# Kernel optimization log

Measured on AMD Instinct MI355X. Metric: run time of the kernel, lower is better.

## Reference

```python
import jax, jax.numpy as jnp
import numpy as np

B, N, D_IN, D_H, D_OUT = 32768, 8, 256, 512, 256
LN_EPS = 1e-5


def setup_inputs() -> dict:
    key = jax.random.key(0)
    ks = jax.random.split(key, 9)
    s = lambda fan_in: 1.0 / np.sqrt(fan_in)
    return {
        "state": jax.random.normal(ks[0], (B, D_IN), dtype=jnp.float32),
        "neighbor_states": jax.random.normal(ks[1], (N, B, D_IN), dtype=jnp.float32),
        "ln_gamma": jnp.ones((D_IN,), jnp.float32),
        "ln_beta": jnp.zeros((D_IN,), jnp.float32),
        "W1": jax.random.uniform(ks[2], (D_IN, D_H), jnp.float32, -s(D_IN), s(D_IN)),
        "b1": jax.random.uniform(ks[3], (D_H,), jnp.float32, -s(D_IN), s(D_IN)),
        "W2": jax.random.uniform(ks[4], (D_H, D_OUT), jnp.float32, -s(D_H), s(D_H)),
        "b2": jax.random.uniform(ks[5], (D_OUT,), jnp.float32, -s(D_H), s(D_H)),
        "attn_w": jax.random.uniform(ks[6], (D_OUT,), jnp.float32, -s(D_OUT), s(D_OUT)),
        "attn_b": jax.random.uniform(ks[7], (), jnp.float32, -s(D_OUT), s(D_OUT)),
    }


def reference(state, neighbor_states, ln_gamma, ln_beta, W1, b1, W2, b2, attn_w, attn_b):
    def process(x):
        # LayerNorm over last dim (eps=1e-5, elementwise affine)
        mu = jnp.mean(x, axis=-1, keepdims=True)
        var = jnp.mean(jnp.square(x - mu), axis=-1, keepdims=True)
        xn = (x - mu) * jax.lax.rsqrt(var + LN_EPS) * ln_gamma + ln_beta
        # Linear -> (Dropout=identity in eval) -> ReLU -> Linear
        h = jax.nn.relu(xn @ W1 + b1)
        return h @ W2 + b2

    local = process(state)                      # [B, D_OUT]
    nf = process(neighbor_states)               # [N, B, D_OUT]
    # attention aggregation: scores over neighbor axis (torch stacks at dim=1)
    scores = jnp.einsum("nbo,o->nb", nf, attn_w) + attn_b   # [N, B]
    weights = jax.nn.softmax(scores, axis=0)                  # softmax over neighbors
    agg = jnp.einsum("nbo,nb->bo", nf, weights)              # [B, D_OUT]
    return local + agg
```

## Files before the change

### kernel.cpp

```cpp
#include <hip/hip_runtime.h>
#include <hip/hip_bf16.h>
#include <math.h>

#define BROWS 32768
#define NNB   8
#define DIN   256
#define DH    512
#define DOUT  256
#define MROWS 128
#define CH    32
#define NCHUNK 16
#define SA    264
#define SH    40

typedef __attribute__((ext_vector_type(8))) short bfrag;
typedef __attribute__((ext_vector_type(4))) float ffrag;
typedef __attribute__((ext_vector_type(4))) float f4v;

__device__ __forceinline__ short f2bf(float f) {
    union { float f; unsigned u; } v; v.f = f;
    unsigned r = v.u + 0x7fffu + ((v.u >> 16) & 1u);
    return (short)(r >> 16);
}

__global__ void tcast_g(const float* __restrict__ src, const float* __restrict__ g,
                        short* __restrict__ dst, int R, int C) {
    __shared__ short t[64][67];
    const int c0 = blockIdx.x * 64, r0 = blockIdx.y * 64;
    const int lr = threadIdx.x >> 6, lc = threadIdx.x & 63;
    #pragma unroll
    for (int i = 0; i < 16; ++i) {
        int row = i * 4 + lr;
        t[row][lc] = f2bf(src[(size_t)(r0 + row) * C + c0 + lc] * g[r0 + row]);
    }
    __syncthreads();
    #pragma unroll
    for (int i = 0; i < 16; ++i) {
        int row = i * 4 + lr;
        dst[(size_t)(c0 + row) * R + r0 + lc] = t[lc][row];
    }
}

__global__ void tcast(const float* __restrict__ src, short* __restrict__ dst,
                      int R, int C) {
    __shared__ short t[64][67];
    const int c0 = blockIdx.x * 64, r0 = blockIdx.y * 64;
    const int lr = threadIdx.x >> 6, lc = threadIdx.x & 63;
    #pragma unroll
    for (int i = 0; i < 16; ++i) {
        int row = i * 4 + lr;
        t[row][lc] = f2bf(src[(size_t)(r0 + row) * C + c0 + lc]);
    }
    __syncthreads();
    #pragma unroll
    for (int i = 0; i < 16; ++i) {
        int row = i * 4 + lr;
        dst[(size_t)(c0 + row) * R + r0 + lc] = t[lc][row];
    }
}

__global__ void b1prep(const float* __restrict__ W1, const float* __restrict__ b1,
                       const float* __restrict__ beta, float* __restrict__ b1p) {
    int n = blockIdx.x * 256 + threadIdx.x;
    float acc = b1[n];
    for (int k = 0; k < DIN; ++k) acc += beta[k] * W1[(size_t)k * DH + n];
    b1p[n] = acc;
}

__global__ __launch_bounds__(512, 2)
void fused_node(const float* __restrict__ state, const float* __restrict__ nbr,
                const float* __restrict__ b1p, const float* __restrict__ b2g,
                const float* __restrict__ awg, const float* __restrict__ abg,
                const short* __restrict__ w1t, const short* __restrict__ w2t,
                float* __restrict__ out) {
    __shared__ short w1_lds[2][CH * SA];
    __shared__ short w2_lds[2][DOUT * SH];
    __shared__ short h_lds[MROWS * SH];
    __shared__ float b1_lds[DH];
    __shared__ float scorep[4 * MROWS];
    __shared__ float m_lds[MROWS], l_lds[MROWS], al_lds[MROWS], pp_lds[MROWS], il_lds[MROWS];

    const int tid = threadIdx.x;
    const int wv = tid >> 6, lane = tid & 63;
    const int q = lane >> 4, l16 = lane & 15;
    const int rg = wv >> 2, cg = wv & 3;
    const int row0 = blockIdx.x * MROWS;
    const int myrow = 16 * wv + l16;

    const int f0 = tid, f1 = tid + 512;
    const int w1r0 = f0 >> 5, w1c0 = f0 & 31, w1r1 = f1 >> 5, w1c1 = f1 & 31;
    const int w2r0 = f0 >> 2, w2c0 = f0 & 3,  w2r1 = f1 >> 2, w2c1 = f1 & 3;

    bfrag L1a = *(const bfrag*)(w1t + (size_t)f0 * 8);
    bfrag L1b = *(const bfrag*)(w1t + (size_t)f1 * 8);
    bfrag L2a = *(const bfrag*)(w2t + (size_t)w2r0 * DH + w2c0 * 8);
    bfrag L2b = *(const bfrag*)(w2t + (size_t)w2r1 * DH + w2c1 * 8);
    if (tid < DH) b1_lds[tid] = b1p[tid];
    if (tid < MROWS) { m_lds[tid] = -__builtin_huge_valf(); l_lds[tid] = 0.f; }
    *(bfrag*)(&w1_lds[0][w1r0 * SA + w1c0 * 8]) = L1a;
    *(bfrag*)(&w1_lds[0][w1r1 * SA + w1c1 * 8]) = L1b;
    *(bfrag*)(&w2_lds[0][w2r0 * SH + w2c0 * 8]) = L2a;
    *(bfrag*)(&w2_lds[0][w2r1 * SH + w2c1 * 8]) = L2b;

    float b2v[4], awv[4];
    #pragma unroll
    for (int ct = 0; ct < 4; ++ct) {
        int col = 64 * cg + 16 * ct + l16;
        b2v[ct] = b2g[col];
        awv[ct] = awg[col];
    }
    const float attnb = abg[0];

    ffrag agg[4][4];
    #pragma unroll
    for (int mt = 0; mt < 4; ++mt)
        #pragma unroll
        for (int ct = 0; ct < 4; ++ct) { ffrag z = {0.f,0.f,0.f,0.f}; agg[mt][ct] = z; }

    ffrag feat[4][4];
    bfrag xnf[8];

    for (int s = 0; s < 9; ++s) {
        const bool loc = (s == 8);
        const float* xb = loc ? (state + (size_t)row0 * DIN)
                              : (nbr + ((size_t)s * BROWS + (size_t)row0) * DIN);
        {
            const float* xr = xb + (size_t)myrow * DIN + q * 8;
            f4v xa[8], xc[8];
            #pragma unroll
            for (int kb = 0; kb < 8; ++kb) {
                xa[kb] = __builtin_nontemporal_load((const f4v*)(xr + kb * 32));
                xc[kb] = __builtin_nontemporal_load((const f4v*)(xr + kb * 32 + 4));
            }
            float sum = 0.f, ssq = 0.f;
            #pragma unroll
            for (int kb = 0; kb < 8; ++kb) {
                #pragma unroll
                for (int j = 0; j < 4; ++j) {
                    sum += xa[kb][j] + xc[kb][j];
                    ssq = fmaf(xa[kb][j], xa[kb][j], fmaf(xc[kb][j], xc[kb][j], ssq));
                }
            }
            sum += __shfl_xor(sum, 16); sum += __shfl_xor(sum, 32);
            ssq += __shfl_xor(ssq, 16); ssq += __shfl_xor(ssq, 32);
            float mean = sum * (1.f / 256.f);
            float var = ssq * (1.f / 256.f) - mean * mean;
            float rstd = rsqrtf(var + 1e-5f);
            #pragma unroll
            for (int kb = 0; kb < 8; ++kb) {
                bfrag t;
                #pragma unroll
                for (int j = 0; j < 4; ++j) {
                    t[j]     = f2bf((xa[kb][j] - mean) * rstd);
                    t[j + 4] = f2bf((xc[kb][j] - mean) * rstd);
                }
                xnf[kb] = t;
            }
        }
        #pragma unroll
        for (int mt = 0; mt < 4; ++mt)
            #pragma unroll
            for (int ct = 0; ct < 4; ++ct) {
                ffrag fi = {b2v[ct], b2v[ct], b2v[ct], b2v[ct]};
                feat[mt][ct] = fi;
            }

        for (int c = 0; c < NCHUNK; ++c) {
            const int p = c & 1;
            __syncthreads();
            const bool more = (c < NCHUNK - 1) || (s < 8);
            const int nc = (c + 1) & (NCHUNK - 1);
            if (more) {
                const short* s1 = w1t + (size_t)nc * CH * DIN;
                const short* s2 = w2t + nc * CH;
                L1a = *(const bfrag*)(s1 + (size_t)f0 * 8);
                L1b = *(const bfrag*)(s1 + (size_t)f1 * 8);
                L2a = *(const bfrag*)(s2 + (size_t)w2r0 * DH + w2c0 * 8);
                L2b = *(const bfrag*)(s2 + (size_t)w2r1 * DH + w2c1 * 8);
            }
            {
                float bb0 = b1_lds[c * CH + l16], bb1 = b1_lds[c * CH + 16 + l16];
                ffrag h0 = {bb0, bb0, bb0, bb0};
                ffrag h1 = {bb1, bb1, bb1, bb1};
                const short* bp = &w1_lds[p][l16 * SA + q * 8];
                #pragma unroll
                for (int kb = 0; kb < 8; ++kb) {
                    bfrag v0 = *(const bfrag*)(bp + kb * 32);
                    bfrag v1 = *(const bfrag*)(bp + 16 * SA + kb * 32);
                    h0 = __builtin_amdgcn_mfma_f32_16x16x32_bf16(xnf[kb], v0, h0, 0, 0, 0);
                    h1 = __builtin_amdgcn_mfma_f32_16x16x32_bf16(xnf[kb], v1, h1, 0, 0, 0);
                }
                short* hb = h_lds + (16 * wv + 4 * q) * SH + l16;
                #pragma unroll
                for (int r = 0; r < 4; ++r) {
                    hb[r * SH]      = f2bf(fmaxf(h0[r], 0.f));
                    hb[r * SH + 16] = f2bf(fmaxf(h1[r], 0.f));
                }
            }
            if (more) {
                *(bfrag*)(&w1_lds[1 - p][w1r0 * SA + w1c0 * 8]) = L1a;
                *(bfrag*)(&w1_lds[1 - p][w1r1 * SA + w1c1 * 8]) = L1b;
                *(bfrag*)(&w2_lds[1 - p][w2r0 * SH + w2c0 * 8]) = L2a;
                *(bfrag*)(&w2_lds[1 - p][w2r1 * SH + w2c1 * 8]) = L2b;
            }
            __syncthreads();
            {
                bfrag af[4], bfr[4];
                #pragma unroll
                for (int mt = 0; mt < 4; ++mt)
                    af[mt] = *(const bfrag*)(h_lds + (64 * rg + 16 * mt + l16) * SH + q * 8);
                #pragma unroll
                for (int ct = 0; ct < 4; ++ct)
                    bfr[ct] = *(const bfrag*)(&w2_lds[p][(64 * cg + 16 * ct + l16) * SH + q * 8]);
                #pragma unroll
                for (int mt = 0; mt < 4; ++mt)
                    #pragma unroll
                    for (int ct = 0; ct < 4; ++ct)
                        feat[mt][ct] = __builtin_amdgcn_mfma_f32_16x16x32_bf16(af[mt], bfr[ct], feat[mt][ct], 0, 0, 0);
            }
        }

        if (!loc) {
            float sp[4][4];
            #pragma unroll
            for (int mt = 0; mt < 4; ++mt)
                #pragma unroll
                for (int r = 0; r < 4; ++r) {
                    float vv = feat[mt][0][r] * awv[0] + feat[mt][1][r] * awv[1]
                             + feat[mt][2][r] * awv[2] + feat[mt][3][r] * awv[3];
                    vv += __shfl_xor(vv, 1); vv += __shfl_xor(vv, 2);
                    vv += __shfl_xor(vv, 4); vv += __shfl_xor(vv, 8);
                    sp[mt][r] = vv;
                }
            if (l16 == 0) {
                #pragma unroll
                for (int mt = 0; mt < 4; ++mt)
                    #pragma unroll
                    for (int r = 0; r < 4; ++r)
                        scorep[cg * MROWS + 64 * rg + 16 * mt + 4 * q + r] = sp[mt][r];
            }
            __syncthreads();
            if (tid < MROWS) {
                float sc = scorep[tid] + scorep[MROWS + tid] + scorep[2 * MROWS + tid]
                         + scorep[3 * MROWS + tid] + attnb;
                float mo = m_lds[tid];
                float mn = fmaxf(mo, sc);
                float al = __expf(mo - mn);
                float pp = __expf(sc - mn);
                float ln = l_lds[tid] * al + pp;
                m_lds[tid] = mn; l_lds[tid] = ln;
                al_lds[tid] = al; pp_lds[tid] = pp;
                if (s == NNB - 1) il_lds[tid] = 1.f / ln;
            }
            __syncthreads();
            #pragma unroll
            for (int mt = 0; mt < 4; ++mt) {
                float alv[4], ppv[4];
                #pragma unroll
                for (int r = 0; r < 4; ++r) {
                    int rr = 64 * rg + 16 * mt + 4 * q + r;
                    alv[r] = al_lds[rr]; ppv[r] = pp_lds[rr];
                }
                #pragma unroll
                for (int ct = 0; ct < 4; ++ct)
                    #pragma unroll
                    for (int r = 0; r < 4; ++r)
                        agg[mt][ct][r] = agg[mt][ct][r] * alv[r] + ppv[r] * feat[mt][ct][r];
            }
        }
    }

    #pragma unroll
    for (int mt = 0; mt < 4; ++mt)
        #pragma unroll
        for (int r = 0; r < 4; ++r) {
            int rr = 64 * rg + 16 * mt + 4 * q + r;
            float il = il_lds[rr];
            size_t base = (size_t)(row0 + rr) * DOUT + 64 * cg + l16;
            #pragma unroll
            for (int ct = 0; ct < 4; ++ct)
                __builtin_nontemporal_store(feat[mt][ct][r] + agg[mt][ct][r] * il,
                                            out + base + ct * 16);
        }
}

extern "C" void kernel_launch(void* const* d_in, const int* in_sizes, int n_in,
                              void* d_out, int out_size, void* d_ws, size_t ws_size,
                              hipStream_t stream) {
    const float* state = (const float*)d_in[0];
    const float* nbr   = (const float*)d_in[1];
    const float* gamma = (const float*)d_in[2];
    const float* beta  = (const float*)d_in[3];
    const float* W1    = (const float*)d_in[4];
    const float* b1    = (const float*)d_in[5];
    const float* W2    = (const float*)d_in[6];
    const float* b2    = (const float*)d_in[7];
    const float* aw    = (const float*)d_in[8];
    const float* ab    = (const float*)d_in[9];
    float* out = (float*)d_out;

    short* w1t = (short*)d_ws;
    short* w2t = w1t + (size_t)DH * DIN;
    float* b1p = (float*)(w2t + (size_t)DOUT * DH);

    tcast_g<<<dim3(DH / 64, DIN / 64), 256, 0, stream>>>(W1, gamma, w1t, DIN, DH);
    tcast<<<dim3(DOUT / 64, DH / 64), 256, 0, stream>>>(W2, w2t, DH, DOUT);
    b1prep<<<2, 256, 0, stream>>>(W1, b1, beta, b1p);
    fused_node<<<BROWS / MROWS, 512, 0, stream>>>(state, nbr, b1p, b2, aw, ab,
                                                  w1t, w2t, out);
}
```

Measured before the change: 636.5 us.

## Aggregate hidden activations before second linear layer using folded attention weights

Folds attn_w through W2, so each score is a dot product of the hidden activation with a precomputed W2·attn_w vector plus a folded bias. The online-softmax aggregation then runs over the 512-wide hidden activations rather than the output features, and the second GEMM runs only once per row on (h_local + weighted hidden sum). This removes eight of nine W2 GEMMs and the W2 streaming from the per-neighbor loop. In exchange it keeps large per-thread hidden accumulators in registers plus hidden activations in LDS, which adds register and LDS pressure and a bf16 rounding of the summed input to the final GEMM. It also uses a swizzled W1 layout in LDS in place of padding.

```diff
diff --git a/kernel.cpp b/kernel.cpp
--- a/kernel.cpp
+++ b/kernel.cpp
@@ -10,8 +10,7 @@
 #define MROWS 128
 #define CH    32
 #define NCHUNK 16
-#define SA    264
-#define SH    40
+#define NCLDS 14
 
 typedef __attribute__((ext_vector_type(8))) short bfrag;
 typedef __attribute__((ext_vector_type(4))) float ffrag;
@@ -21,6 +20,11 @@
     union { float f; unsigned u; } v; v.f = f;
     unsigned r = v.u + 0x7fffu + ((v.u >> 16) & 1u);
     return (short)(r >> 16);
+}
+__device__ __forceinline__ float bf2f(short s) {
+    union { float f; unsigned u; } v;
+    v.u = ((unsigned)(unsigned short)s) << 16;
+    return v.f;
 }
 
 __global__ void tcast_g(const float* __restrict__ src, const float* __restrict__ g,
@@ -67,65 +71,67 @@
     b1p[n] = acc;
 }
 
+__global__ void w2aprep(const float* __restrict__ W2, const float* __restrict__ aw,
+                        const float* __restrict__ ab, const float* __restrict__ b2,
+                        float* __restrict__ w2a) {
+    int h = threadIdx.x;
+    float acc = 0.f;
+    for (int o = 0; o < DOUT; ++o) acc += W2[(size_t)h * DOUT + o] * aw[o];
+    w2a[h] = acc;
+    if (h == 0) {
+        float s = ab[0];
+        for (int o = 0; o < DOUT; ++o) s += b2[o] * aw[o];
+        w2a[DH] = s;
+    }
+}
+
 __global__ __launch_bounds__(512, 2)
 void fused_node(const float* __restrict__ state, const float* __restrict__ nbr,
-                const float* __restrict__ b1p, const float* __restrict__ b2g,
-                const float* __restrict__ awg, const float* __restrict__ abg,
+                const float* __restrict__ b1p, const float* __restrict__ b2,
+                const float* __restrict__ w2a_g,
                 const short* __restrict__ w1t, const short* __restrict__ w2t,
                 float* __restrict__ out) {
-    __shared__ short w1_lds[2][CH * SA];
-    __shared__ short w2_lds[2][DOUT * SH];
-    __shared__ short h_lds[MROWS * SH];
+    __shared__ short w1buf[2][CH * DIN];
+    __shared__ short h_s[NCLDS * 512 * 8];
     __shared__ float b1_lds[DH];
-    __shared__ float scorep[4 * MROWS];
+    __shared__ float w2a_lds[DH + 1];
+    __shared__ float scorep[2 * MROWS];
     __shared__ float m_lds[MROWS], l_lds[MROWS], al_lds[MROWS], pp_lds[MROWS], il_lds[MROWS];
 
     const int tid = threadIdx.x;
     const int wv = tid >> 6, lane = tid & 63;
     const int q = lane >> 4, l16 = lane & 15;
-    const int rg = wv >> 2, cg = wv & 3;
+    const int rg2 = wv >> 1, cg = wv & 1;
     const int row0 = blockIdx.x * MROWS;
-    const int myrow = 16 * wv + l16;
-
-    const int f0 = tid, f1 = tid + 512;
-    const int w1r0 = f0 >> 5, w1c0 = f0 & 31, w1r1 = f1 >> 5, w1c1 = f1 & 31;
-    const int w2r0 = f0 >> 2, w2c0 = f0 & 3,  w2r1 = f1 >> 2, w2c1 = f1 & 3;
-
-    bfrag L1a = *(const bfrag*)(w1t + (size_t)f0 * 8);
-    bfrag L1b = *(const bfrag*)(w1t + (size_t)f1 * 8);
-    bfrag L2a = *(const bfrag*)(w2t + (size_t)w2r0 * DH + w2c0 * 8);
-    bfrag L2b = *(const bfrag*)(w2t + (size_t)w2r1 * DH + w2c1 * 8);
-    if (tid < DH) b1_lds[tid] = b1p[tid];
+
+    const int t0 = tid, t1 = tid + 512;
+    const int g0 = ((t0 >> 5) << 5) | ((t0 & 31) ^ ((t0 >> 5) & 7));
+    const int g1 = ((t1 >> 5) << 5) | ((t1 & 31) ^ ((t1 >> 5) & 7));
+
+    if (tid < DH) { b1_lds[tid] = b1p[tid]; w2a_lds[tid] = w2a_g[tid]; }
+    if (tid == 0) w2a_lds[DH] = w2a_g[DH];
     if (tid < MROWS) { m_lds[tid] = -__builtin_huge_valf(); l_lds[tid] = 0.f; }
-    *(bfrag*)(&w1_lds[0][w1r0 * SA + w1c0 * 8]) = L1a;
-    *(bfrag*)(&w1_lds[0][w1r1 * SA + w1c1 * 8]) = L1b;
-    *(bfrag*)(&w2_lds[0][w2r0 * SH + w2c0 * 8]) = L2a;
-    *(bfrag*)(&w2_lds[0][w2r1 * SH + w2c1 * 8]) = L2b;
-
-    float b2v[4], awv[4];
-    #pragma unroll
-    for (int ct = 0; ct < 4; ++ct) {
-        int col = 64 * cg + 16 * ct + l16;
-        b2v[ct] = b2g[col];
-        awv[ct] = awg[col];
-    }
-    const float attnb = abg[0];
-
-    ffrag agg[4][4];
-    #pragma unroll
-    for (int mt = 0; mt < 4; ++mt)
-        #pragma unroll
-        for (int ct = 0; ct < 4; ++ct) { ffrag z = {0.f,0.f,0.f,0.f}; agg[mt][ct] = z; }
-
-    ffrag feat[4][4];
-    bfrag xnf[8];
-
-    for (int s = 0; s < 9; ++s) {
-        const bool loc = (s == 8);
-        const float* xb = loc ? (state + (size_t)row0 * DIN)
-                              : (nbr + ((size_t)s * BROWS + (size_t)row0) * DIN);
-        {
-            const float* xr = xb + (size_t)myrow * DIN + q * 8;
+
+    bfrag P0 = *(const bfrag*)(w1t + (size_t)g0 * 8);
+    bfrag P1 = *(const bfrag*)(w1t + (size_t)g1 * 8);
+    *(bfrag*)(&w1buf[0][t0 * 8]) = P0;
+    *(bfrag*)(&w1buf[0][t1 * 8]) = P1;
+
+    float hbar[NCHUNK][8];
+    #pragma unroll
+    for (int c = 0; c < NCHUNK; ++c)
+        #pragma unroll
+        for (int j = 0; j < 8; ++j) hbar[c][j] = 0.f;
+
+    bfrag hreg14, hreg15;
+    bfrag xnf[2][8];
+
+    for (int s = 0; s <= NNB; ++s) {
+        const float* xb = (s == NNB) ? (state + (size_t)row0 * DIN)
+                                     : (nbr + ((size_t)s * BROWS + (size_t)row0) * DIN);
+        #pragma unroll
+        for (int rf = 0; rf < 2; ++rf) {
+            const float* xr = xb + (size_t)(32 * rg2 + 16 * rf + l16) * DIN + q * 8;
             f4v xa[8], xc[8];
             #pragma unroll
             for (int kb = 0; kb < 8; ++kb) {
@@ -134,13 +140,12 @@
             }
             float sum = 0.f, ssq = 0.f;
             #pragma unroll
-            for (int kb = 0; kb < 8; ++kb) {
+            for (int kb = 0; kb < 8; ++kb)
                 #pragma unroll
                 for (int j = 0; j < 4; ++j) {
                     sum += xa[kb][j] + xc[kb][j];
                     ssq = fmaf(xa[kb][j], xa[kb][j], fmaf(xc[kb][j], xc[kb][j], ssq));
                 }
-            }
             sum += __shfl_xor(sum, 16); sum += __shfl_xor(sum, 32);
             ssq += __shfl_xor(ssq, 16); ssq += __shfl_xor(ssq, 32);
             float mean = sum * (1.f / 256.f);
@@ -154,95 +159,72 @@
                     t[j]     = f2bf((xa[kb][j] - mean) * rstd);
                     t[j + 4] = f2bf((xc[kb][j] - mean) * rstd);
                 }
-                xnf[kb] = t;
-            }
-        }
-        #pragma unroll
-        for (int mt = 0; mt < 4; ++mt)
-            #pragma unroll
-            for (int ct = 0; ct < 4; ++ct) {
-                ffrag fi = {b2v[ct], b2v[ct], b2v[ct], b2v[ct]};
-                feat[mt][ct] = fi;
-            }
+                xnf[rf][kb] = t;
+            }
+            __builtin_amdgcn_sched_barrier(0);
+        }
+
+        float sp0[4] = {0.f, 0.f, 0.f, 0.f}, sp1[4] = {0.f, 0.f, 0.f, 0.f};
 
         for (int c = 0; c < NCHUNK; ++c) {
             const int p = c & 1;
             __syncthreads();
-            const bool more = (c < NCHUNK - 1) || (s < 8);
-            const int nc = (c + 1) & (NCHUNK - 1);
+            const bool more = (c < NCHUNK - 1) || (s < NNB);
             if (more) {
-                const short* s1 = w1t + (size_t)nc * CH * DIN;
-                const short* s2 = w2t + nc * CH;
-                L1a = *(const bfrag*)(s1 + (size_t)f0 * 8);
-                L1b = *(const bfrag*)(s1 + (size_t)f1 * 8);
-                L2a = *(const bfrag*)(s2 + (size_t)w2r0 * DH + w2c0 * 8);
-                L2b = *(const bfrag*)(s2 + (size_t)w2r1 * DH + w2c1 * 8);
-            }
-            {
-                float bb0 = b1_lds[c * CH + l16], bb1 = b1_lds[c * CH + 16 + l16];
-                ffrag h0 = {bb0, bb0, bb0, bb0};
-                ffrag h1 = {bb1, bb1, bb1, bb1};
-                const short* bp = &w1_lds[p][l16 * SA + q * 8];
-                #pragma unroll
-                for (int kb = 0; kb < 8; ++kb) {
-                    bfrag v0 = *(const bfrag*)(bp + kb * 32);
-                    bfrag v1 = *(const bfrag*)(bp + 16 * SA + kb * 32);
-                    h0 = __builtin_amdgcn_mfma_f32_16x16x32_bf16(xnf[kb], v0, h0, 0, 0, 0);
-                    h1 = __builtin_amdgcn_mfma_f32_16x16x32_bf16(xnf[kb], v1, h1, 0, 0, 0);
-                }
-                short* hb = h_lds + (16 * wv + 4 * q) * SH + l16;
+                const short* sb = w1t + (size_t)((c + 1) & (NCHUNK - 1)) * (CH * DIN);
+                P0 = *(const bfrag*)(sb + g0 * 8);
+                P1 = *(const bfrag*)(sb + g1 * 8);
+            }
+            const int col = c * CH + 16 * cg + l16;
+            const float bb = b1_lds[col];
+            const float w2av = w2a_lds[col];
+            ffrag h0 = {bb, bb, bb, bb}, h1 = {bb, bb, bb, bb};
+            const short* bp = &w1buf[p][(16 * cg + l16) * DIN];
+            const int e7 = l16 & 7;
+            #pragma unroll
+            for (int kb = 0; kb < 8; ++kb) {
+                bfrag w = *(const bfrag*)(bp + (((kb * 4 + q) ^ e7) << 3));
+                h0 = __builtin_amdgcn_mfma_f32_16x16x32_bf16(xnf[0][kb], w, h0, 0, 0, 0);
+                h1 = __builtin_amdgcn_mfma_f32_16x16x32_bf16(xnf[1][kb], w, h1, 0, 0, 0);
+            }
+            bfrag hb;
+            #pragma unroll
+            for (int r = 0; r < 4; ++r) {
+                float v0 = fmaxf(h0[r], 0.f), v1 = fmaxf(h1[r], 0.f);
+                sp0[r] += v0 * w2av; sp1[r] += v1 * w2av;
+                hb[r] = f2bf(v0); hb[r + 4] = f2bf(v1);
+            }
+            if (c < NCLDS) *(bfrag*)(h_s + ((size_t)(c * 512 + tid) * 8)) = hb;
+            else if (c == 14) hreg14 = hb;
+            else hreg15 = hb;
+            if (more) {
+                *(bfrag*)(&w1buf[1 - p][t0 * 8]) = P0;
+                *(bfrag*)(&w1buf[1 - p][t1 * 8]) = P1;
+            }
+        }
+
+        if (s < NNB) {
+            #pragma unroll
+            for (int r = 0; r < 4; ++r) {
+                float v = sp0[r];
+                v += __shfl_xor(v, 1); v += __shfl_xor(v, 2);
+                v += __shfl_xor(v, 4); v += __shfl_xor(v, 8);
+                sp0[r] = v;
+                v = sp1[r];
+                v += __shfl_xor(v, 1); v += __shfl_xor(v, 2);
+                v += __shfl_xor(v, 4); v += __shfl_xor(v, 8);
+                sp1[r] = v;
+            }
+            if (l16 == 0) {
                 #pragma unroll
                 for (int r = 0; r < 4; ++r) {
-                    hb[r * SH]      = f2bf(fmaxf(h0[r], 0.f));
-                    hb[r * SH + 16] = f2bf(fmaxf(h1[r], 0.f));
+                    scorep[cg * MROWS + 32 * rg2 + 4 * q + r]      = sp0[r];
+                    scorep[cg * MROWS + 32 * rg2 + 16 + 4 * q + r] = sp1[r];
                 }
-            }
-            if (more) {
-                *(bfrag*)(&w1_lds[1 - p][w1r0 * SA + w1c0 * 8]) = L1a;
-                *(bfrag*)(&w1_lds[1 - p][w1r1 * SA + w1c1 * 8]) = L1b;
-                *(bfrag*)(&w2_lds[1 - p][w2r0 * SH + w2c0 * 8]) = L2a;
-                *(bfrag*)(&w2_lds[1 - p][w2r1 * SH + w2c1 * 8]) = L2b;
-            }
-            __syncthreads();
-            {
-                bfrag af[4], bfr[4];
-                #pragma unroll
-                for (int mt = 0; mt < 4; ++mt)
-                    af[mt] = *(const bfrag*)(h_lds + (64 * rg + 16 * mt + l16) * SH + q * 8);
-                #pragma unroll
-                for (int ct = 0; ct < 4; ++ct)
-                    bfr[ct] = *(const bfrag*)(&w2_lds[p][(64 * cg + 16 * ct + l16) * SH + q * 8]);
-                #pragma unroll
-                for (int mt = 0; mt < 4; ++mt)
-                    #pragma unroll
-                    for (int ct = 0; ct < 4; ++ct)
-                        feat[mt][ct] = __builtin_amdgcn_mfma_f32_16x16x32_bf16(af[mt], bfr[ct], feat[mt][ct], 0, 0, 0);
-            }
-        }
-
-        if (!loc) {
-            float sp[4][4];
-            #pragma unroll
-            for (int mt = 0; mt < 4; ++mt)
-                #pragma unroll
-                for (int r = 0; r < 4; ++r) {
-                    float vv = feat[mt][0][r] * awv[0] + feat[mt][1][r] * awv[1]
-                             + feat[mt][2][r] * awv[2] + feat[mt][3][r] * awv[3];
-                    vv += __shfl_xor(vv, 1); vv += __shfl_xor(vv, 2);
-                    vv += __shfl_xor(vv, 4); vv += __shfl_xor(vv, 8);
-                    sp[mt][r] = vv;
-                }
-            if (l16 == 0) {
-                #pragma unroll
-                for (int mt = 0; mt < 4; ++mt)
-                    #pragma unroll
-                    for (int r = 0; r < 4; ++r)
-                        scorep[cg * MROWS + 64 * rg + 16 * mt + 4 * q + r] = sp[mt][r];
             }
             __syncthreads();
             if (tid < MROWS) {
-                float sc = scorep[tid] + scorep[MROWS + tid] + scorep[2 * MROWS + tid]
-                         + scorep[3 * MROWS + tid] + attnb;
+                float sc = scorep[tid] + scorep[MROWS + tid] + w2a_lds[DH];
                 float mo = m_lds[tid];
                 float mn = fmaxf(mo, sc);
                 float al = __expf(mo - mn);
@@ -253,34 +235,79 @@
                 if (s == NNB - 1) il_lds[tid] = 1.f / ln;
             }
             __syncthreads();
-            #pragma unroll
-            for (int mt = 0; mt < 4; ++mt) {
-                float alv[4], ppv[4];
+            float al8[8], pp8[8];
+            #pragma unroll
+            for (int j = 0; j < 8; ++j) {
+                int rr = 32 * rg2 + 16 * (j >> 2) + 4 * q + (j & 3);
+                al8[j] = al_lds[rr]; pp8[j] = pp_lds[rr];
+            }
+            #pragma unroll
+            for (int c = 0; c < NCHUNK; ++c) {
+                bfrag hb = (c < NCLDS)
+                             ? *(const bfrag*)(h_s + ((size_t)(c * 512 + tid) * 8))
+                             : (c == 14 ? hreg14 : hreg15);
                 #pragma unroll
-                for (int r = 0; r < 4; ++r) {
-                    int rr = 64 * rg + 16 * mt + 4 * q + r;
-                    alv[r] = al_lds[rr]; ppv[r] = pp_lds[rr];
-                }
-                #pragma unroll
-                for (int ct = 0; ct < 4; ++ct)
-                    #pragma unroll
-                    for (int r = 0; r < 4; ++r)
-                        agg[mt][ct][r] = agg[mt][ct][r] * alv[r] + ppv[r] * feat[mt][ct][r];
-            }
-        }
-    }
-
+                for (int j = 0; j < 8; ++j)
+                    hbar[c][j] = al8[j] * hbar[c][j] + pp8[j] * bf2f(hb[j]);
+                if ((c & 3) == 3) __builtin_amdgcn_sched_barrier(0);
+            }
+        }
+    }
+
+    __syncthreads();
+    short* a_lds = &w1buf[0][0];
+    float il8[8];
+    #pragma unroll
+    for (int j = 0; j < 8; ++j)
+        il8[j] = il_lds[32 * rg2 + 16 * (j >> 2) + 4 * q + (j & 3)];
+    const int rg = wv >> 2, cg2 = wv & 3;
+    float b2v[4];
+    #pragma unroll
+    for (int ct = 0; ct < 4; ++ct) b2v[ct] = 2.f * b2[64 * cg2 + 16 * ct + l16];
+    ffrag feat[4][4];
     #pragma unroll
     for (int mt = 0; mt < 4; ++mt)
         #pragma unroll
+        for (int ct = 0; ct < 4; ++ct) {
+            ffrag fi = {b2v[ct], b2v[ct], b2v[ct], b2v[ct]};
+            feat[mt][ct] = fi;
+        }
+    const int akey = (q ^ (l16 >> 2)) << 3;
+    #pragma unroll
+    for (int c = 0; c < NCHUNK; ++c) {
+        bfrag hl = (c < NCLDS)
+                     ? *(const bfrag*)(h_s + ((size_t)(c * 512 + tid) * 8))
+                     : (c == 14 ? hreg14 : hreg15);
+        #pragma unroll
+        for (int j = 0; j < 8; ++j) {
+            int row = 32 * rg2 + 16 * (j >> 2) + 4 * q + (j & 3);
+            int cswz = ((((16 * cg + l16) >> 3) ^ ((row >> 2) & 3)) << 3) | (l16 & 7);
+            a_lds[row * 40 + cswz] = f2bf(bf2f(hl[j]) + hbar[c][j] * il8[j]);
+        }
+        __syncthreads();
+        bfrag af[4], bfr[4];
+        #pragma unroll
+        for (int mt = 0; mt < 4; ++mt)
+            af[mt] = *(const bfrag*)(a_lds + (64 * rg + 16 * mt + l16) * 40 + akey);
+        #pragma unroll
+        for (int ct = 0; ct < 4; ++ct)
+            bfr[ct] = *(const bfrag*)(w2t + (size_t)(64 * cg2 + 16 * ct + l16) * DH + c * CH + q * 8);
+        #pragma unroll
+        for (int mt = 0; mt < 4; ++mt)
+            #pragma unroll
+            for (int ct = 0; ct < 4; ++ct)
+                feat[mt][ct] = __builtin_amdgcn_mfma_f32_16x16x32_bf16(af[mt], bfr[ct], feat[mt][ct], 0, 0, 0);
+        __syncthreads();
+    }
+    #pragma unroll
+    for (int mt = 0; mt < 4; ++mt)
+        #pragma unroll
         for (int r = 0; r < 4; ++r) {
-            int rr = 64 * rg + 16 * mt + 4 * q + r;
-            float il = il_lds[rr];
-            size_t base = (size_t)(row0 + rr) * DOUT + 64 * cg + l16;
+            int row = 64 * rg + 16 * mt + 4 * q + r;
+            size_t base = (size_t)(row0 + row) * DOUT + 64 * cg2 + l16;
             #pragma unroll
             for (int ct = 0; ct < 4; ++ct)
-                __builtin_nontemporal_store(feat[mt][ct][r] + agg[mt][ct][r] * il,
-                                            out + base + ct * 16);
+                __builtin_nontemporal_store(feat[mt][ct][r], out + base + ct * 16);
         }
 }
 
@@ -302,10 +329,12 @@
     short* w1t = (short*)d_ws;
     short* w2t = w1t + (size_t)DH * DIN;
     float* b1p = (float*)(w2t + (size_t)DOUT * DH);
+    float* w2a = b1p + DH;
 
     tcast_g<<<dim3(DH / 64, DIN / 64), 256, 0, stream>>>(W1, gamma, w1t, DIN, DH);
     tcast<<<dim3(DOUT / 64, DH / 64), 256, 0, stream>>>(W2, w2t, DH, DOUT);
     b1prep<<<2, 256, 0, stream>>>(W1, b1, beta, b1p);
-    fused_node<<<BROWS / MROWS, 512, 0, stream>>>(state, nbr, b1p, b2, aw, ab,
+    w2aprep<<<1, 512, 0, stream>>>(W2, aw, ab, b2, w2a);
+    fused_node<<<BROWS / MROWS, 512, 0, stream>>>(state, nbr, b1p, b2, w2a,
                                                   w1t, w2t, out);
 }
```

New measurement: 989.1 us. +55.4%, slower.

## Restructure fused MLP: full hidden tile in LDS, direct weight loads, prefetch next input

Applied to the files above, without the earlier changes.

The kernel now computes the whole 128x512 hidden activation for a source into one large swizzled LDS buffer. W1 and W2 fragments are read straight from global/L2, in a W1 layout pre-packed per chunk, instead of being double-buffered through LDS with a barrier every chunk. The next source's input rows are loaded and LayerNorm statistics accumulated while the second GEMM and the softmax update run, which cuts the barriers per source and hides input-load latency. In exchange it uses much more LDS (about 147KB), which may limit occupancy. It also quantises inputs to bf16 before normalisation, adding a little rounding error.

```diff
diff --git a/kernel.cpp b/kernel.cpp
--- a/kernel.cpp
+++ b/kernel.cpp
@@ -10,8 +10,6 @@
 #define MROWS 128
 #define CH    32
 #define NCHUNK 16
-#define SA    264
-#define SH    40
 
 typedef __attribute__((ext_vector_type(8))) short bfrag;
 typedef __attribute__((ext_vector_type(4))) float ffrag;
@@ -22,22 +20,27 @@
     unsigned r = v.u + 0x7fffu + ((v.u >> 16) & 1u);
     return (short)(r >> 16);
 }
-
-__global__ void tcast_g(const float* __restrict__ src, const float* __restrict__ g,
-                        short* __restrict__ dst, int R, int C) {
-    __shared__ short t[64][67];
-    const int c0 = blockIdx.x * 64, r0 = blockIdx.y * 64;
-    const int lr = threadIdx.x >> 6, lc = threadIdx.x & 63;
-    #pragma unroll
-    for (int i = 0; i < 16; ++i) {
-        int row = i * 4 + lr;
-        t[row][lc] = f2bf(src[(size_t)(r0 + row) * C + c0 + lc] * g[r0 + row]);
-    }
-    __syncthreads();
-    #pragma unroll
-    for (int i = 0; i < 16; ++i) {
-        int row = i * 4 + lr;
-        dst[(size_t)(c0 + row) * R + r0 + lc] = t[lc][row];
+__device__ __forceinline__ float bf2f(short s) {
+    union { float f; unsigned u; } v;
+    v.u = ((unsigned)(unsigned short)s) << 16;
+    return v.f;
+}
+
+__global__ void w1prep(const float* __restrict__ W1, const float* __restrict__ g,
+                       short* __restrict__ dst) {
+    const int c = blockIdx.x;
+    const int t = threadIdx.x;
+    #pragma unroll
+    for (int i = 0; i < 4; ++i) {
+        int f = t + 256 * i;
+        int j = f >> 5, r = f & 31;
+        bfrag v;
+        #pragma unroll
+        for (int e = 0; e < 8; ++e) {
+            int k = j * 8 + e;
+            v[e] = f2bf(W1[(size_t)k * DH + 32 * c + r] * g[k]);
+        }
+        *(bfrag*)(dst + (size_t)c * 8192 + (size_t)f * 8) = v;
     }
 }
 
@@ -67,15 +70,48 @@
     b1p[n] = acc;
 }
 
-__global__ __launch_bounds__(512, 2)
+__device__ __forceinline__ void ln_load_rf(const float* __restrict__ xr,
+                                           bfrag* dst, float& sum_o, float& ssq_o) {
+    float sum = 0.f, ssq = 0.f;
+    #pragma unroll
+    for (int k2 = 0; k2 < 8; ++k2) {
+        f4v xa = __builtin_nontemporal_load((const f4v*)(xr + k2 * 32));
+        f4v xc = __builtin_nontemporal_load((const f4v*)(xr + k2 * 32 + 4));
+        bfrag t;
+        #pragma unroll
+        for (int j = 0; j < 4; ++j) {
+            sum += xa[j] + xc[j];
+            ssq = fmaf(xa[j], xa[j], fmaf(xc[j], xc[j], ssq));
+            t[j]     = f2bf(xa[j]);
+            t[j + 4] = f2bf(xc[j]);
+        }
+        dst[k2] = t;
+    }
+    sum_o = sum; ssq_o = ssq;
+}
+
+__device__ __forceinline__ void ln_finish_rf(bfrag* x8, float sum, float ssq) {
+    sum += __shfl_xor(sum, 16); sum += __shfl_xor(sum, 32);
+    ssq += __shfl_xor(ssq, 16); ssq += __shfl_xor(ssq, 32);
+    float mean = sum * (1.f / 256.f);
+    float var = ssq * (1.f / 256.f) - mean * mean;
+    float rstd = rsqrtf(var + 1e-5f);
+    #pragma unroll
+    for (int kb = 0; kb < 8; ++kb) {
+        bfrag t = x8[kb];
+        #pragma unroll
+        for (int j = 0; j < 8; ++j) t[j] = f2bf((bf2f(t[j]) - mean) * rstd);
+        x8[kb] = t;
+    }
+}
+
+__global__ __launch_bounds__(512) __attribute__((amdgpu_waves_per_eu(2, 2)))
 void fused_node(const float* __restrict__ state, const float* __restrict__ nbr,
-                const float* __restrict__ b1p, const float* __restrict__ b2g,
-                const float* __restrict__ awg, const float* __restrict__ abg,
+                const float* __restrict__ b1p, const float* __restrict__ b2,
+                const float* __restrict__ aw, const float* __restrict__ ab,
                 const short* __restrict__ w1t, const short* __restrict__ w2t,
                 float* __restrict__ out) {
-    __shared__ short w1_lds[2][CH * SA];
-    __shared__ short w2_lds[2][DOUT * SH];
-    __shared__ short h_lds[MROWS * SH];
+    __shared__ short h_all[8 * 128 * 72];
     __shared__ float b1_lds[DH];
     __shared__ float scorep[4 * MROWS];
     __shared__ float m_lds[MROWS], l_lds[MROWS], al_lds[MROWS], pp_lds[MROWS], il_lds[MROWS];
@@ -83,80 +119,47 @@
     const int tid = threadIdx.x;
     const int wv = tid >> 6, lane = tid & 63;
     const int q = lane >> 4, l16 = lane & 15;
-    const int rg = wv >> 2, cg = wv & 3;
+    const int rg2 = wv >> 1, cg = wv & 1;
+    const int rg  = wv >> 2, cg2 = wv & 3;
     const int row0 = blockIdx.x * MROWS;
-    const int myrow = 16 * wv + l16;
-
-    const int f0 = tid, f1 = tid + 512;
-    const int w1r0 = f0 >> 5, w1c0 = f0 & 31, w1r1 = f1 >> 5, w1c1 = f1 & 31;
-    const int w2r0 = f0 >> 2, w2c0 = f0 & 3,  w2r1 = f1 >> 2, w2c1 = f1 & 3;
-
-    bfrag L1a = *(const bfrag*)(w1t + (size_t)f0 * 8);
-    bfrag L1b = *(const bfrag*)(w1t + (size_t)f1 * 8);
-    bfrag L2a = *(const bfrag*)(w2t + (size_t)w2r0 * DH + w2c0 * 8);
-    bfrag L2b = *(const bfrag*)(w2t + (size_t)w2r1 * DH + w2c1 * 8);
-    if (tid < DH) b1_lds[tid] = b1p[tid];
+
+    b1_lds[tid] = b1p[tid];
     if (tid < MROWS) { m_lds[tid] = -__builtin_huge_valf(); l_lds[tid] = 0.f; }
-    *(bfrag*)(&w1_lds[0][w1r0 * SA + w1c0 * 8]) = L1a;
-    *(bfrag*)(&w1_lds[0][w1r1 * SA + w1c1 * 8]) = L1b;
-    *(bfrag*)(&w2_lds[0][w2r0 * SH + w2c0 * 8]) = L2a;
-    *(bfrag*)(&w2_lds[0][w2r1 * SH + w2c1 * 8]) = L2b;
 
     float b2v[4], awv[4];
     #pragma unroll
     for (int ct = 0; ct < 4; ++ct) {
-        int col = 64 * cg + 16 * ct + l16;
-        b2v[ct] = b2g[col];
-        awv[ct] = awg[col];
-    }
-    const float attnb = abg[0];
+        b2v[ct] = b2[64 * cg2 + 16 * ct + l16];
+        awv[ct] = aw[64 * cg2 + 16 * ct + l16];
+    }
+    const float attnb = ab[0];
+
+    const int cw  = (((2 * cg + (l16 >> 3)) ^ q) << 3) | (l16 & 7);
+    const int rb1 = 32 * rg2 + 4 * q;
+    const short* wbase = w1t + (16 * cg + l16) * 8 + q * 256;
+    const int arow = 64 * rg + l16;
+    const int akx  = (q ^ (l16 >> 2)) << 3;
 
     ffrag agg[4][4];
     #pragma unroll
     for (int mt = 0; mt < 4; ++mt)
         #pragma unroll
-        for (int ct = 0; ct < 4; ++ct) { ffrag z = {0.f,0.f,0.f,0.f}; agg[mt][ct] = z; }
-
+        for (int ct = 0; ct < 4; ++ct) { ffrag z = {0.f, 0.f, 0.f, 0.f}; agg[mt][ct] = z; }
+
+    bfrag xnf[2][8];
+    float sums[2], ssqs[2];
     ffrag feat[4][4];
-    bfrag xnf[8];
-
-    for (int s = 0; s < 9; ++s) {
-        const bool loc = (s == 8);
-        const float* xb = loc ? (state + (size_t)row0 * DIN)
-                              : (nbr + ((size_t)s * BROWS + (size_t)row0) * DIN);
-        {
-            const float* xr = xb + (size_t)myrow * DIN + q * 8;
-            f4v xa[8], xc[8];
-            #pragma unroll
-            for (int kb = 0; kb < 8; ++kb) {
-                xa[kb] = __builtin_nontemporal_load((const f4v*)(xr + kb * 32));
-                xc[kb] = __builtin_nontemporal_load((const f4v*)(xr + kb * 32 + 4));
-            }
-            float sum = 0.f, ssq = 0.f;
-            #pragma unroll
-            for (int kb = 0; kb < 8; ++kb) {
-                #pragma unroll
-                for (int j = 0; j < 4; ++j) {
-                    sum += xa[kb][j] + xc[kb][j];
-                    ssq = fmaf(xa[kb][j], xa[kb][j], fmaf(xc[kb][j], xc[kb][j], ssq));
-                }
-            }
-            sum += __shfl_xor(sum, 16); sum += __shfl_xor(sum, 32);
-            ssq += __shfl_xor(ssq, 16); ssq += __shfl_xor(ssq, 32);
-            float mean = sum * (1.f / 256.f);
-            float var = ssq * (1.f / 256.f) - mean * mean;
-            float rstd = rsqrtf(var + 1e-5f);
-            #pragma unroll
-            for (int kb = 0; kb < 8; ++kb) {
-                bfrag t;
-                #pragma unroll
-                for (int j = 0; j < 4; ++j) {
-                    t[j]     = f2bf((xa[kb][j] - mean) * rstd);
-                    t[j + 4] = f2bf((xc[kb][j] - mean) * rstd);
-                }
-                xnf[kb] = t;
-            }
-        }
+
+    {
+        const float* xb = nbr + (size_t)row0 * DIN;
+        ln_load_rf(xb + (size_t)(32 * rg2 + l16) * DIN + q * 8, xnf[0], sums[0], ssqs[0]);
+        ln_load_rf(xb + (size_t)(32 * rg2 + 16 + l16) * DIN + q * 8, xnf[1], sums[1], ssqs[1]);
+        ln_finish_rf(xnf[0], sums[0], ssqs[0]);
+        ln_finish_rf(xnf[1], sums[1], ssqs[1]);
+    }
+    __syncthreads();
+
+    for (int s = 0; s <= NNB; ++s) {
         #pragma unroll
         for (int mt = 0; mt < 4; ++mt)
             #pragma unroll
@@ -164,63 +167,51 @@
                 ffrag fi = {b2v[ct], b2v[ct], b2v[ct], b2v[ct]};
                 feat[mt][ct] = fi;
             }
-
         for (int c = 0; c < NCHUNK; ++c) {
-            const int p = c & 1;
-            __syncthreads();
-            const bool more = (c < NCHUNK - 1) || (s < 8);
-            const int nc = (c + 1) & (NCHUNK - 1);
-            if (more) {
-                const short* s1 = w1t + (size_t)nc * CH * DIN;
-                const short* s2 = w2t + nc * CH;
-                L1a = *(const bfrag*)(s1 + (size_t)f0 * 8);
-                L1b = *(const bfrag*)(s1 + (size_t)f1 * 8);
-                L2a = *(const bfrag*)(s2 + (size_t)w2r0 * DH + w2c0 * 8);
-                L2b = *(const bfrag*)(s2 + (size_t)w2r1 * DH + w2c1 * 8);
-            }
-            {
-                float bb0 = b1_lds[c * CH + l16], bb1 = b1_lds[c * CH + 16 + l16];
-                ffrag h0 = {bb0, bb0, bb0, bb0};
-                ffrag h1 = {bb1, bb1, bb1, bb1};
-                const short* bp = &w1_lds[p][l16 * SA + q * 8];
-                #pragma unroll
-                for (int kb = 0; kb < 8; ++kb) {
-                    bfrag v0 = *(const bfrag*)(bp + kb * 32);
-                    bfrag v1 = *(const bfrag*)(bp + 16 * SA + kb * 32);
-                    h0 = __builtin_amdgcn_mfma_f32_16x16x32_bf16(xnf[kb], v0, h0, 0, 0, 0);
-                    h1 = __builtin_amdgcn_mfma_f32_16x16x32_bf16(xnf[kb], v1, h1, 0, 0, 0);
-                }
-                short* hb = h_lds + (16 * wv + 4 * q) * SH + l16;
-                #pragma unroll
-                for (int r = 0; r < 4; ++r) {
-                    hb[r * SH]      = f2bf(fmaxf(h0[r], 0.f));
-                    hb[r * SH + 16] = f2bf(fmaxf(h1[r], 0.f));
-                }
-            }
-            if (more) {
-                *(bfrag*)(&w1_lds[1 - p][w1r0 * SA + w1c0 * 8]) = L1a;
-                *(bfrag*)(&w1_lds[1 - p][w1r1 * SA + w1c1 * 8]) = L1b;
-                *(bfrag*)(&w2_lds[1 - p][w2r0 * SH + w2c0 * 8]) = L2a;
-                *(bfrag*)(&w2_lds[1 - p][w2r1 * SH + w2c1 * 8]) = L2b;
-            }
-            __syncthreads();
-            {
-                bfrag af[4], bfr[4];
-                #pragma unroll
-                for (int mt = 0; mt < 4; ++mt)
-                    af[mt] = *(const bfrag*)(h_lds + (64 * rg + 16 * mt + l16) * SH + q * 8);
+            const short* wp = wbase + c * 8192;
+            const float bb = b1_lds[c * 32 + 16 * cg + l16];
+            ffrag h0 = {bb, bb, bb, bb}, h1 = {bb, bb, bb, bb};
+            #pragma unroll
+            for (int kb = 0; kb < 8; ++kb) {
+                bfrag w = *(const bfrag*)(wp + kb * 1024);
+                h0 = __builtin_amdgcn_mfma_f32_16x16x32_bf16(xnf[0][kb], w, h0, 0, 0, 0);
+                h1 = __builtin_amdgcn_mfma_f32_16x16x32_bf16(xnf[1][kb], w, h1, 0, 0, 0);
+            }
+            short* hp = h_all + (c >> 1) * 9216 + (c & 1) * 32 + cw;
+            #pragma unroll
+            for (int r = 0; r < 4; ++r) {
+                hp[(rb1 + r) * 72]      = f2bf(fmaxf(h0[r], 0.f));
+                hp[(rb1 + 16 + r) * 72] = f2bf(fmaxf(h1[r], 0.f));
+            }
+        }
+        __syncthreads();
+
+        const bool more = (s < NNB);
+        const float* xbn = nullptr;
+        if (more) {
+            xbn = (s + 1 == NNB) ? (state + (size_t)row0 * DIN)
+                                 : (nbr + ((size_t)(s + 1) * BROWS + (size_t)row0) * DIN);
+            ln_load_rf(xbn + (size_t)(32 * rg2 + l16) * DIN + q * 8, xnf[0], sums[0], ssqs[0]);
+        }
+
+        for (int c = 0; c < NCHUNK; ++c) {
+            const short* hq = h_all + (c >> 1) * 9216 + (c & 1) * 32 + akx;
+            bfrag af[4], bfr[4];
+            #pragma unroll
+            for (int mt = 0; mt < 4; ++mt)
+                af[mt] = *(const bfrag*)(hq + (arow + 16 * mt) * 72);
+            #pragma unroll
+            for (int ct = 0; ct < 4; ++ct)
+                bfr[ct] = *(const bfrag*)(w2t + (size_t)(64 * cg2 + 16 * ct + l16) * DH + c * 32 + q * 8);
+            #pragma unroll
+            for (int mt = 0; mt < 4; ++mt)
                 #pragma unroll
                 for (int ct = 0; ct < 4; ++ct)
-                    bfr[ct] = *(const bfrag*)(&w2_lds[p][(64 * cg + 16 * ct + l16) * SH + q * 8]);
-                #pragma unroll
-                for (int mt = 0; mt < 4; ++mt)
-                    #pragma unroll
-                    for (int ct = 0; ct < 4; ++ct)
-                        feat[mt][ct] = __builtin_amdgcn_mfma_f32_16x16x32_bf16(af[mt], bfr[ct], feat[mt][ct], 0, 0, 0);
-            }
-        }
-
-        if (!loc) {
+                    feat[mt][ct] = __builtin_amdgcn_mfma_f32_16x16x32_bf16(af[mt], bfr[ct], feat[mt][ct], 0, 0, 0);
+        }
+
+        if (more) {
+            ln_load_rf(xbn + (size_t)(32 * rg2 + 16 + l16) * DIN + q * 8, xnf[1], sums[1], ssqs[1]);
             float sp[4][4];
             #pragma unroll
             for (int mt = 0; mt < 4; ++mt)
@@ -237,7 +228,7 @@
                 for (int mt = 0; mt < 4; ++mt)
                     #pragma unroll
                     for (int r = 0; r < 4; ++r)
-                        scorep[cg * MROWS + 64 * rg + 16 * mt + 4 * q + r] = sp[mt][r];
+                        scorep[cg2 * MROWS + 64 * rg + 16 * mt + 4 * q + r] = sp[mt][r];
             }
             __syncthreads();
             if (tid < MROWS) {
@@ -267,6 +258,8 @@
                     for (int r = 0; r < 4; ++r)
                         agg[mt][ct][r] = agg[mt][ct][r] * alv[r] + ppv[r] * feat[mt][ct][r];
             }
+            ln_finish_rf(xnf[0], sums[0], ssqs[0]);
+            ln_finish_rf(xnf[1], sums[1], ssqs[1]);
         }
     }
 
@@ -274,9 +267,9 @@
     for (int mt = 0; mt < 4; ++mt)
         #pragma unroll
         for (int r = 0; r < 4; ++r) {
-            int rr = 64 * rg + 16 * mt + 4 * q + r;
-            float il = il_lds[rr];
-            size_t base = (size_t)(row0 + rr) * DOUT + 64 * cg + l16;
+            int row = 64 * rg + 16 * mt + 4 * q + r;
+            float il = il_lds[row];
+            size_t base = (size_t)(row0 + row) * DOUT + 64 * cg2 + l16;
             #pragma unroll
             for (int ct = 0; ct < 4; ++ct)
                 __builtin_nontemporal_store(feat[mt][ct][r] + agg[mt][ct][r] * il,
@@ -303,7 +296,7 @@
     short* w2t = w1t + (size_t)DH * DIN;
     float* b1p = (float*)(w2t + (size_t)DOUT * DH);
 
-    tcast_g<<<dim3(DH / 64, DIN / 64), 256, 0, stream>>>(W1, gamma, w1t, DIN, DH);
+    w1prep<<<NCHUNK, 256, 0, stream>>>(W1, gamma, w1t);
     tcast<<<dim3(DOUT / 64, DH / 64), 256, 0, stream>>>(W2, w2t, DH, DOUT);
     b1prep<<<2, 256, 0, stream>>>(W1, b1, beta, b1p);
     fused_node<<<BROWS / MROWS, 512, 0, stream>>>(state, nbr, b1p, b2, aw, ab,
```

Result: slower. 1.042 ms (+63.7%).
